# Kernel optimization log

Measured on AMD Instinct MI355X. Metric: run time of the kernel, lower is better.

Reference implementation:

```python
import jax, jax.numpy as jnp
import numpy as np

B, S, D = 2, 2048, 1024
H, DK = 16, 64
NUM_BUCKETS, MAX_DIST = 32, 128
EPS = 1e-6


def _relative_position_bucket(q_len, k_len):
    # T5 bidirectional relative position bucketing.
    ctx = jnp.arange(q_len)[:, None]
    mem = jnp.arange(k_len)[None, :]
    rel = mem - ctx  # [q, k]
    nb = NUM_BUCKETS // 2
    ret = (rel > 0).astype(jnp.int32) * nb
    n = jnp.abs(rel)
    max_exact = nb // 2
    is_small = n < max_exact
    n_safe = jnp.maximum(n, 1).astype(jnp.float32)
    val_large = max_exact + (
        jnp.log(n_safe / max_exact) / np.log(MAX_DIST / max_exact) * (nb - max_exact)
    ).astype(jnp.int32)
    val_large = jnp.minimum(val_large, nb - 1)
    return ret + jnp.where(is_small, n, val_large)  # [q, k] int32


def setup_inputs() -> dict:
    key = jax.random.key(0)
    ks = jax.random.split(key, 7)
    s = 0.02
    return {
        "hidden_states": jax.random.normal(ks[0], (B, S, D), jnp.float32),
        "ln_g": jnp.ones((D,), jnp.float32),
        "ln_b": jnp.zeros((D,), jnp.float32),
        "Wq": jax.random.normal(ks[1], (D, H * DK), jnp.float32) * s,
        "Wk": jax.random.normal(ks[2], (D, H * DK), jnp.float32) * s,
        "Wv": jax.random.normal(ks[3], (D, H * DK), jnp.float32) * s,
        "Wo": jax.random.normal(ks[4], (H * DK, D), jnp.float32) * s,
        "rel_bias": jax.random.normal(ks[5], (NUM_BUCKETS, H), jnp.float32) * s,
    }


def reference(hidden_states, ln_g, ln_b, Wq, Wk, Wv, Wo, rel_bias):
    b, s, d = hidden_states.shape
    # LayerNorm (nn.LayerNorm with affine, biased variance)
    mu = jnp.mean(hidden_states, axis=-1, keepdims=True)
    var = jnp.mean(jnp.square(hidden_states - mu), axis=-1, keepdims=True)
    normed = (hidden_states - mu) * jax.lax.rsqrt(var + EPS) * ln_g + ln_b
    # QKV projections (no bias), split heads
    q = (normed @ Wq).reshape(b, s, H, DK)
    k = (normed @ Wk).reshape(b, s, H, DK)
    v = (normed @ Wv).reshape(b, s, H, DK)
    # T5 attention: NO 1/sqrt(d) scaling; learned relative-position bias added to logits
    scores = jnp.einsum("bqhd,bkhd->bhqk", q, k)
    bucket = _relative_position_bucket(s, s)          # [s, s]
    bias = jnp.transpose(rel_bias[bucket], (2, 0, 1))  # [H, s, s]
    attn = jax.nn.softmax(scores + bias[None], axis=-1)
    ctx = jnp.einsum("bhqk,bkhd->bqhd", attn, v).reshape(b, s, H * DK)
    out = ctx @ Wo
    # residual (dropout is identity in eval)
    return hidden_states + out
```

## Files before the change

### kernel.cpp

```cpp
#include <hip/hip_runtime.h>
#include <hip/hip_bf16.h>
#include <math.h>

typedef __attribute__((__ext_vector_type__(8))) short bf16x8;
typedef __attribute__((__ext_vector_type__(4))) float f32x4;
typedef __attribute__((__ext_vector_type__(16))) float f32x16;
typedef __attribute__((__ext_vector_type__(4))) unsigned int u32x4;

#define B_ 2
#define S_ 2048
#define D_ 1024
#define H_ 16
#define DK_ 64
#define M_ (B_*S_)
#define N3_ 3072
#define BIAS_LEN 4096
#define M0_ 24.0f
#define L2E_ 1.4426950408889634f
#define KSTRIDE 66

__device__ __forceinline__ unsigned int cvtpk(float a, float b){
  unsigned int r;
  asm("v_cvt_pk_bf16_f32 %0, %1, %2" : "=v"(r) : "v"(a), "v"(b));
  return r;
}
__device__ __forceinline__ unsigned short f2bf(float f){
  unsigned int r;
  asm("v_cvt_pk_bf16_f32 %0, %1, %2" : "=v"(r) : "v"(f), "v"(f));
  return (unsigned short)r;
}
__device__ __forceinline__ float bf2f(unsigned short u){
  union{unsigned int i; float f;} v; v.i = ((unsigned int)u)<<16; return v.f;
}

__device__ __forceinline__ float fexp2(float x){
#if __has_builtin(__builtin_amdgcn_exp2f)
  return __builtin_amdgcn_exp2f(x);
#else
  return __expf(x * 0.6931471805599453f);
#endif
}

__device__ __forceinline__ f32x4 zero4(){
  f32x4 z; z[0]=0.f; z[1]=0.f; z[2]=0.f; z[3]=0.f; return z;
}

__device__ __forceinline__ f32x4 mfma16(bf16x8 a, bf16x8 b, f32x4 c){
  return __builtin_amdgcn_mfma_f32_16x16x32_bf16(a, b, c, 0, 0, 0);
}
__device__ __forceinline__ f32x16 mfma32(bf16x8 a, bf16x8 b, f32x16 c){
  return __builtin_amdgcn_mfma_f32_32x32x16_bf16(a, b, c, 0, 0, 0);
}

__device__ __forceinline__ void gload16(const void* g, void* l){
  __builtin_amdgcn_global_load_lds(
      (const __attribute__((address_space(1))) void*)g,
      (__attribute__((address_space(3))) void*)l, 16, 0, 0);
}

__global__ __launch_bounds__(256) void transpose_cast_kernel(
    const float* __restrict__ Wq, const float* __restrict__ Wk,
    const float* __restrict__ Wv, const float* __restrict__ Wo,
    unsigned short* __restrict__ Wcat_t, unsigned short* __restrict__ Wo_t)
{
  __shared__ float tile[64][65];
  const int k0 = blockIdx.x * 64;
  const int v0 = blockIdx.y * 64;
  const int sel = v0 >> 10;
  const float* W = (sel==0) ? Wq : (sel==1) ? Wk : (sel==2) ? Wv : Wo;
  const int nn0 = v0 & 1023;
  #pragma unroll
  for (int i=0;i<16;i++){
    int idx = i*256 + threadIdx.x;
    int r = idx >> 6, c = idx & 63;
    tile[r][c] = W[(size_t)(k0+r)*1024 + nn0 + c];
  }
  __syncthreads();
  #pragma unroll
  for (int i=0;i<16;i++){
    int idx = i*256 + threadIdx.x;
    int nr = idx >> 6, kc = idx & 63;
    unsigned short bv = f2bf(tile[kc][nr]);
    if (sel < 3) Wcat_t[(size_t)(v0+nr)*1024 + k0 + kc] = bv;
    else         Wo_t[(size_t)(v0-3072+nr)*1024 + k0 + kc] = bv;
  }
}

__global__ __launch_bounds__(256) void bias_tab_kernel(
    const float* __restrict__ rel_bias, float* __restrict__ biasTab)
{
  int t = blockIdx.x*256 + threadIdx.x;
  if (t >= H_*BIAS_LEN) return;
  int h = t / BIAS_LEN;
  int idx = t - h*BIAS_LEN;
  int rel = idx - (S_-1);
  int ret = (rel > 0) ? 16 : 0;
  int n = (rel < 0) ? -rel : rel;
  int bidx;
  if (n < 8) bidx = n;
  else {
    float vl = logf((float)n * 0.125f) / 2.7725887f * 8.0f;
    int v = 8 + (int)vl;
    bidx = (v < 15) ? v : 15;
  }
  biasTab[t] = (rel_bias[(ret + bidx)*H_ + h] - M0_) * L2E_;
}

__global__ __launch_bounds__(256) void ln_kernel(
    const float* __restrict__ x, const float* __restrict__ g,
    const float* __restrict__ bta, unsigned short* __restrict__ out)
{
  const int row = blockIdx.x;
  const int tid = threadIdx.x;
  float4 v = ((const float4*)(x + (size_t)row*D_))[tid];
  float s  = v.x+v.y+v.z+v.w;
  float ss = v.x*v.x+v.y*v.y+v.z*v.z+v.w*v.w;
  #pragma unroll
  for (int off=1; off<64; off<<=1){ s += __shfl_xor(s,off,64); ss += __shfl_xor(ss,off,64); }
  __shared__ float rs[4], rss[4];
  const int wid = tid >> 6, lane = tid & 63;
  if (lane == 0){ rs[wid] = s; rss[wid] = ss; }
  __syncthreads();
  s  = rs[0]+rs[1]+rs[2]+rs[3];
  ss = rss[0]+rss[1]+rss[2]+rss[3];
  float mu  = s * (1.0f/1024.0f);
  float var = ss * (1.0f/1024.0f) - mu*mu;
  float rstd = rsqrtf(var + 1e-6f);
  float4 gg = ((const float4*)g)[tid];
  float4 bb = ((const float4*)bta)[tid];
  uint2 o;
  o.x = cvtpk((v.x-mu)*rstd*gg.x + bb.x, (v.y-mu)*rstd*gg.y + bb.y);
  o.y = cvtpk((v.z-mu)*rstd*gg.z + bb.z, (v.w-mu)*rstd*gg.w + bb.w);
  ((uint2*)(out + (size_t)row*D_))[tid] = o;
}

template<int MODE>
__global__ __launch_bounds__(256) void gemm_kernel(
    const unsigned short* __restrict__ A,
    const unsigned short* __restrict__ Bt,
    const float* __restrict__ resid,
    unsigned short* __restrict__ Qb,
    unsigned short* __restrict__ Kb,
    unsigned short* __restrict__ Vtb,
    float* __restrict__ outf,
    int Ndim, int Kdim)
{
  __shared__ unsigned short As[128*64];
  __shared__ unsigned short Bs[128*64];
  const int tid = threadIdx.x;
  const int wid = tid >> 6, lane = tid & 63;
  const int lr = lane & 15, lg = lane >> 4;
  const int wm = (wid >> 1) * 64, wn = (wid & 1) * 64;

  const int nbx = gridDim.x;
  const int total = nbx * gridDim.y;
  const int flat = blockIdx.y * nbx + blockIdx.x;
  const int swz = (flat & 7) * (total >> 3) + (flat >> 3);
  const int m0 = (swz % nbx) * 128, n0 = (swz / nbx) * 128;

  f32x4 acc[4][4];
  #pragma unroll
  for (int i=0;i<4;i++)
    #pragma unroll
    for (int j=0;j<4;j++) acc[i][j] = zero4();

  for (int k0 = 0; k0 < Kdim; k0 += 64) {
    __syncthreads();
    #pragma unroll
    for (int i=0;i<4;i++){
      int c = i*256 + tid;
      int row = c >> 3, ch = c & 7;
      int chs = ch ^ (row & 7);
      gload16(A  + (size_t)(m0+row)*Kdim + k0 + chs*8, As + c*8);
      gload16(Bt + (size_t)(n0+row)*Kdim + k0 + chs*8, Bs + c*8);
    }
    __syncthreads();
    #pragma unroll
    for (int kk=0;kk<2;kk++){
      bf16x8 aF[4], bF[4];
      #pragma unroll
      for (int mi=0;mi<4;mi++){
        int row = wm + mi*16 + lr;
        aF[mi] = *(const bf16x8*)&As[row*64 + (((kk*4+lg) ^ (row & 7)) * 8)];
      }
      #pragma unroll
      for (int ni=0;ni<4;ni++){
        int row = wn + ni*16 + lr;
        bF[ni] = *(const bf16x8*)&Bs[row*64 + (((kk*4+lg) ^ (row & 7)) * 8)];
      }
      #pragma unroll
      for (int mi=0;mi<4;mi++)
        #pragma unroll
        for (int ni=0;ni<4;ni++)
          acc[mi][ni] = mfma16(aF[mi], bF[ni], acc[mi][ni]);
    }
  }

  if (MODE == 1) {
    #pragma unroll
    for (int mi=0;mi<4;mi++)
      #pragma unroll
      for (int ni=0;ni<4;ni++)
        #pragma unroll
        for (int r=0;r<4;r++){
          int m = m0 + wm + mi*16 + lg*4 + r;
          int n = n0 + wn + ni*16 + lr;
          outf[(size_t)m*Ndim + n] = acc[mi][ni][r] + resid[(size_t)m*Ndim + n];
        }
  } else {
    const int seln = n0 >> 10;
    if (seln == 2) {
      #pragma unroll
      for (int mi=0;mi<4;mi++)
        #pragma unroll
        for (int ni=0;ni<4;ni++){
          int m = m0 + wm + mi*16 + lg*4;
          int n = n0 + wn + ni*16 + lr;
          int nn = n & 1023, hh = nn >> 6, dk = nn & 63;
          int b = m >> 11, s = m & 2047;
          uint2 u;
          u.x = cvtpk(acc[mi][ni][0], acc[mi][ni][1]);
          u.y = cvtpk(acc[mi][ni][2], acc[mi][ni][3]);
          *(uint2*)(Vtb + (((size_t)(b*H_+hh))*DK_ + dk)*S_ + s) = u;
        }
    } else {
      unsigned short* __restrict__ dst = (seln == 0) ? Qb : Kb;
      #pragma unroll
      for (int mi=0;mi<4;mi++)
        #pragma unroll
        for (int ni=0;ni<4;ni++)
          #pragma unroll
          for (int r=0;r<4;r++){
            int m = m0 + wm + mi*16 + lg*4 + r;
            int n = n0 + wn + ni*16 + lr;
            int nn = n & 1023, hh = nn >> 6, dk = nn & 63;
            int b = m >> 11, s = m & 2047;
            dst[(((size_t)(b*H_+hh))*S_ + s)*DK_ + dk] = f2bf(acc[mi][ni][r]);
          }
    }
  }
}

#define SOFTMAX_PV(Svec, BG, UNIP, UNIN, VF00, VF01, VF10, VF11, ACC, LS)        \
{                                                                                \
  float p[16];                                                                   \
  if (UNIP) {                                                                    \
    _Pragma("unroll")                                                            \
    for (int r=0;r<16;r++) p[r] = fexp2(__builtin_fmaf(Svec[r], L2E_, cpos));    \
  } else if (UNIN) {                                                             \
    _Pragma("unroll")                                                            \
    for (int r=0;r<16;r++) p[r] = fexp2(__builtin_fmaf(Svec[r], L2E_, cneg));    \
  } else {                                                                       \
    _Pragma("unroll")                                                            \
    for (int r=0;r<16;r++){                                                      \
      int key = k0 + st*32 + (r&3) + 8*(r>>2) + 4*hi;                            \
      p[r] = fexp2(__builtin_fmaf(Svec[r], L2E_, BG[key]));                      \
    }                                                                            \
  }                                                                              \
                                       \
  {                                                                              \
    float t0=p[0]+p[1], t1=p[2]+p[3], t2=p[4]+p[5], t3=p[6]+p[7];                \
    float t4=p[8]+p[9], t5=p[10]+p[11], t6=p[12]+p[13], t7=p[14]+p[15];          \
    LS += ((t0+t1)+(t2+t3)) + ((t4+t5)+(t6+t7));                                 \
  }                                                                              \
  unsigned int W00=cvtpk(p[0],p[1]),  W01=cvtpk(p[4],p[5]);                      \
  unsigned int W02=cvtpk(p[8],p[9]),  W03=cvtpk(p[12],p[13]);                    \
  unsigned int W10=cvtpk(p[2],p[3]),  W11=cvtpk(p[6],p[7]);                      \
  unsigned int W12=cvtpk(p[10],p[11]),W13=cvtpk(p[14],p[15]);                    \
  unsigned int X00=__shfl_xor(W00,32), X01=__shfl_xor(W01,32);                   \
  unsigned int X02=__shfl_xor(W02,32), X03=__shfl_xor(W03,32);                   \
  unsigned int X10=__shfl_xor(W10,32), X11=__shfl_xor(W11,32);                   \
  unsigned int X12=__shfl_xor(W12,32), X13=__shfl_xor(W13,32);                   \
  u32x4 pu0; u32x4 pu1;                                                          \
  pu0[0] = hi ? X01 : W00;  pu0[1] = hi ? X11 : W10;                             \
  pu0[2] = hi ? W01 : X00;  pu0[3] = hi ? W11 : X10;                             \
  pu1[0] = hi ? X03 : W02;  pu1[1] = hi ? X13 : W12;                             \
  pu1[2] = hi ? W03 : X02;  pu1[3] = hi ? W13 : X12;                             \
  bf16x8 pav0 = __builtin_bit_cast(bf16x8, pu0);                                 \
  bf16x8 pav1 = __builtin_bit_cast(bf16x8, pu1);                                 \
  ACC[0] = mfma32(pav0, VF00, ACC[0]);                                           \
  ACC[1] = mfma32(pav0, VF01, ACC[1]);                                           \
  ACC[0] = mfma32(pav1, VF10, ACC[0]);                                           \
  ACC[1] = mfma32(pav1, VF11, ACC[1]);                                           \
}

__global__ __launch_bounds__(256, 2) void attn_kernel(
    const unsigned short* __restrict__ Qb,
    const unsigned short* __restrict__ Kb,
    const unsigned short* __restrict__ Vtb,
    const float* __restrict__ biasTab,
    const float* __restrict__ rel_bias,
    unsigned short* __restrict__ Opart,
    float* __restrict__ Lpart)
{
  __shared__ unsigned short Ks[64*KSTRIDE];
  __shared__ unsigned short Vts[64*KSTRIDE];

  const int tid = threadIdx.x;
  const int wid = tid >> 6, lane = tid & 63;
  const int ql = lane & 31;
  const int hi = lane >> 5;

  const int flat = (blockIdx.z * 32 + blockIdx.y) * 8 + blockIdx.x;
  const int wf = (flat & 7) * 64 + (flat >> 3);
  const int qt = wf & 7;
  const int bh = (wf >> 3) & 31;
  const int kg = wf >> 8;

  const int h = bh & (H_-1);
  const int b = bh >> 4;
  const int kbase = kg << 10;
  const int q0w = qt*256 + wid*64;

  const float cpos = (rel_bias[31*H_ + h] - M0_) * L2E_;
  const float cneg = (rel_bias[15*H_ + h] - M0_) * L2E_;
  const float* bGa = biasTab + (size_t)h*BIAS_LEN + 2047 - (q0w + ql);
  const float* bGb = bGa - 32;

  const unsigned short* Qpa = Qb + ((size_t)bh*S_ + q0w + ql)*DK_;
  bf16x8 qfa[4], qfb[4];
  #pragma unroll
  for (int c=0;c<4;c++){
    qfa[c] = *(const bf16x8*)(Qpa + 16*c + 8*hi);
    qfb[c] = *(const bf16x8*)(Qpa + 32*DK_ + 16*c + 8*hi);
  }

  const unsigned short* Ksrc = Kb  + (size_t)bh*S_*DK_;
  const unsigned short* Vsrc = Vtb + (size_t)bh*DK_*S_;
  const int c0 = tid, c1 = tid + 256;
  const int r0 = c0 >> 3, ch0 = c0 & 7;
  const int r1 = c1 >> 3, ch1 = c1 & 7;

  f32x16 acca[2], accb[2];
  #pragma unroll
  for (int i=0;i<16;i++){ acca[0][i]=0.f; acca[1][i]=0.f; accb[0][i]=0.f; accb[1][i]=0.f; }
  float lsa = 0.f, lsb = 0.f;

  bf16x8 sk0 = *(const bf16x8*)(Ksrc + (size_t)(kbase + r0)*DK_ + ch0*8);
  bf16x8 sk1 = *(const bf16x8*)(Ksrc + (size_t)(kbase + r1)*DK_ + ch1*8);
  bf16x8 sv0 = *(const bf16x8*)(Vsrc + (size_t)r0*S_ + kbase + ch0*8);
  bf16x8 sv1 = *(const bf16x8*)(Vsrc + (size_t)r1*S_ + kbase + ch1*8);

  for (int k0 = kbase; k0 < kbase + 1024; k0 += 64) {
    __syncthreads();
    *(bf16x8*)&Ks [r0*KSTRIDE + ch0*8] = sk0;
    *(bf16x8*)&Ks [r1*KSTRIDE + ch1*8] = sk1;
    *(bf16x8*)&Vts[r0*KSTRIDE + ch0*8] = sv0;
    *(bf16x8*)&Vts[r1*KSTRIDE + ch1*8] = sv1;
    __syncthreads();
    if (k0 + 64 < kbase + 1024) {
      int kn = k0 + 64;
      sk0 = *(const bf16x8*)(Ksrc + (size_t)(kn + r0)*DK_ + ch0*8);
      sk1 = *(const bf16x8*)(Ksrc + (size_t)(kn + r1)*DK_ + ch1*8);
      sv0 = *(const bf16x8*)(Vsrc + (size_t)r0*S_ + kn + ch0*8);
      sv1 = *(const bf16x8*)(Vsrc + (size_t)r1*S_ + kn + ch1*8);
    }

    const bool upa = (k0 >= q0w + 122),      una = (k0 <= q0w - 154);
    const bool upb = (k0 >= q0w + 32 + 122), unb = (k0 <= q0w + 32 - 154);

    #pragma unroll
    for (int st=0; st<2; ++st){
      const int arow = st*32 + ql;
      bf16x8 kf0 = *(const bf16x8*)&Ks[arow*KSTRIDE + (0+hi)*8];
      bf16x8 kf1 = *(const bf16x8*)&Ks[arow*KSTRIDE + (2+hi)*8];
      bf16x8 kf2 = *(const bf16x8*)&Ks[arow*KSTRIDE + (4+hi)*8];
      bf16x8 kf3 = *(const bf16x8*)&Ks[arow*KSTRIDE + (6+hi)*8];

      f32x16 sa, sb;
      #pragma unroll
      for (int i=0;i<16;i++){ sa[i]=0.f; sb[i]=0.f; }
      sa = mfma32(kf0, qfa[0], sa); sb = mfma32(kf0, qfb[0], sb);
      sa = mfma32(kf1, qfa[1], sa); sb = mfma32(kf1, qfb[1], sb);
      sa = mfma32(kf2, qfa[2], sa); sb = mfma32(kf2, qfb[2], sb);
      sa = mfma32(kf3, qfa[3], sa); sb = mfma32(kf3, qfb[3], sb);

      bf16x8 vf00 = *(const bf16x8*)&Vts[(ql     )*KSTRIDE + (4*st+  hi)*8];
      bf16x8 vf01 = *(const bf16x8*)&Vts[(ql + 32)*KSTRIDE + (4*st+  hi)*8];
      bf16x8 vf10 = *(const bf16x8*)&Vts[(ql     )*KSTRIDE + (4*st+2+hi)*8];
      bf16x8 vf11 = *(const bf16x8*)&Vts[(ql + 32)*KSTRIDE + (4*st+2+hi)*8];

      SOFTMAX_PV(sa, bGa, upa, una, vf00, vf01, vf10, vf11, acca, lsa);
      SOFTMAX_PV(sb, bGb, upb, unb, vf00, vf01, vf10, vf11, accb, lsb);
    }
  }

  float lta = lsa + __shfl_xor(lsa, 32);
  float ltb = lsb + __shfl_xor(lsb, 32);
  if (hi == 0) {
    Lpart[((size_t)kg*B_*H_ + bh)*S_ + q0w + ql]      = lta;
    Lpart[((size_t)kg*B_*H_ + bh)*S_ + q0w + 32 + ql] = ltb;
  }
  #pragma unroll
  for (int r=0;r<16;r++){
    const int qr = (r&3) + 8*(r>>2) + 4*hi;
    #pragma unroll
    for (int dt=0; dt<2; ++dt){
      const int d = ql + 32*dt;
      Opart[(size_t)kg*M_*D_ + ((size_t)(b*S_ + q0w + qr)*H_ + h)*DK_ + d]      = f2bf(acca[dt][r]);
      Opart[(size_t)kg*M_*D_ + ((size_t)(b*S_ + q0w + 32 + qr)*H_ + h)*DK_ + d] = f2bf(accb[dt][r]);
    }
  }
}

__global__ __launch_bounds__(256) void combine_kernel(
    const unsigned short* __restrict__ Opart, const float* __restrict__ Lpart,
    unsigned short* __restrict__ ctxb)
{
  const int t = blockIdx.x*256 + threadIdx.x;
  const int f = t*8;
  const int qgl = f >> 10;
  const int h = (f >> 6) & 15;
  const int bh = (qgl >> 11)*H_ + h;
  const int s = qgl & 2047;
  const float l0 = Lpart[(size_t)bh*S_ + s];
  const float l1 = Lpart[(size_t)B_*H_*S_ + (size_t)bh*S_ + s];
  const float linv = 1.0f / (l0 + l1);
  bf16x8 p0 = *(const bf16x8*)(Opart + f);
  bf16x8 p1 = *(const bf16x8*)(Opart + (size_t)M_*D_ + f);
  u32x4 o;
  #pragma unroll
  for (int j=0;j<4;j++){
    float a = (bf2f((unsigned short)p0[2*j+0]) + bf2f((unsigned short)p1[2*j+0])) * linv;
    float c = (bf2f((unsigned short)p0[2*j+1]) + bf2f((unsigned short)p1[2*j+1])) * linv;
    o[j] = cvtpk(a, c);
  }
  *(u32x4*)(ctxb + f) = o;
}

extern "C" void kernel_launch(void* const* d_in, const int* in_sizes, int n_in,
                              void* d_out, int out_size, void* d_ws, size_t ws_size,
                              hipStream_t stream) {
  const float* hidden   = (const float*)d_in[0];
  const float* ln_g     = (const float*)d_in[1];
  const float* ln_b     = (const float*)d_in[2];
  const float* Wq       = (const float*)d_in[3];
  const float* Wk       = (const float*)d_in[4];
  const float* Wv       = (const float*)d_in[5];
  const float* Wo       = (const float*)d_in[6];
  const float* rel_bias = (const float*)d_in[7];
  float* out = (float*)d_out;

  char* ws = (char*)d_ws;
  const size_t off_ln   = 0;
  const size_t off_wcat = 8388608;
  const size_t off_q    = 16777216;
  const size_t off_k    = 25165824;
  const size_t off_vt   = 33554432;
  const size_t off_ctx  = 41943040;
  const size_t off_bias = 50331648;
  const size_t off_lp   = 50593792;
  const size_t off_wo   = 51118080;

  unsigned short* ln_out  = (unsigned short*)(ws + off_ln);
  unsigned short* Wcat_t  = (unsigned short*)(ws + off_wcat);
  unsigned short* Wo_t    = (unsigned short*)(ws + off_wo);
  unsigned short* Qb      = (unsigned short*)(ws + off_q);
  unsigned short* Kb      = (unsigned short*)(ws + off_k);
  unsigned short* Vtb     = (unsigned short*)(ws + off_vt);
  unsigned short* ctxb    = (unsigned short*)(ws + off_ctx);
  float*          biasTab = (float*)(ws + off_bias);
  float*          Lpart   = (float*)(ws + off_lp);
  unsigned short* Opart   = (unsigned short*)(ws + 0);

  transpose_cast_kernel<<<dim3(16,64), 256, 0, stream>>>(Wq, Wk, Wv, Wo, Wcat_t, Wo_t);
  bias_tab_kernel<<<(H_*BIAS_LEN + 255)/256, 256, 0, stream>>>(rel_bias, biasTab);
  ln_kernel<<<M_, 256, 0, stream>>>(hidden, ln_g, ln_b, ln_out);
  gemm_kernel<0><<<dim3(M_/128, N3_/128), 256, 0, stream>>>(
      ln_out, Wcat_t, nullptr, Qb, Kb, Vtb, nullptr, N3_, D_);
  attn_kernel<<<dim3(8, 32, 2), 256, 0, stream>>>(
      Qb, Kb, Vtb, biasTab, rel_bias, Opart, Lpart);
  combine_kernel<<<(M_*D_/8)/256, 256, 0, stream>>>(Opart, Lpart, ctxb);
  gemm_kernel<1><<<dim3(M_/128, D_/128), 256, 0, stream>>>(
      ctxb, Wo_t, hidden, nullptr, nullptr, nullptr, out, D_, D_);
}
```

Baseline: 141.6 us.

## Fuse split-K attention combine into output projection GEMM A-tile load

```diff
diff --git a/kernel.cpp b/kernel.cpp
--- a/kernel.cpp
+++ b/kernel.cpp
@@ -134,16 +134,12 @@
   ((uint2*)(out + (size_t)row*D_))[tid] = o;
 }
 
-template<int MODE>
-__global__ __launch_bounds__(256) void gemm_kernel(
+__global__ __launch_bounds__(256) void gemm_qkv_kernel(
     const unsigned short* __restrict__ A,
     const unsigned short* __restrict__ Bt,
-    const float* __restrict__ resid,
     unsigned short* __restrict__ Qb,
     unsigned short* __restrict__ Kb,
-    unsigned short* __restrict__ Vtb,
-    float* __restrict__ outf,
-    int Ndim, int Kdim)
+    unsigned short* __restrict__ Vtb)
 {
   __shared__ unsigned short As[128*64];
   __shared__ unsigned short Bs[128*64];
@@ -164,15 +160,15 @@
     #pragma unroll
     for (int j=0;j<4;j++) acc[i][j] = zero4();
 
-  for (int k0 = 0; k0 < Kdim; k0 += 64) {
+  for (int k0 = 0; k0 < D_; k0 += 64) {
     __syncthreads();
     #pragma unroll
     for (int i=0;i<4;i++){
       int c = i*256 + tid;
       int row = c >> 3, ch = c & 7;
       int chs = ch ^ (row & 7);
-      gload16(A  + (size_t)(m0+row)*Kdim + k0 + chs*8, As + c*8);
-      gload16(Bt + (size_t)(n0+row)*Kdim + k0 + chs*8, Bs + c*8);
+      gload16(A  + (size_t)(m0+row)*D_ + k0 + chs*8, As + c*8);
+      gload16(Bt + (size_t)(n0+row)*D_ + k0 + chs*8, Bs + c*8);
     }
     __syncthreads();
     #pragma unroll
@@ -196,7 +192,23 @@
     }
   }
 
-  if (MODE == 1) {
+  const int seln = n0 >> 10;
+  if (seln == 2) {
+    #pragma unroll
+    for (int mi=0;mi<4;mi++)
+      #pragma unroll
+      for (int ni=0;ni<4;ni++){
+        int m = m0 + wm + mi*16 + lg*4;
+        int n = n0 + wn + ni*16 + lr;
+        int nn = n & 1023, hh = nn >> 6, dk = nn & 63;
+        int b = m >> 11, s = m & 2047;
+        uint2 u;
+        u.x = cvtpk(acc[mi][ni][0], acc[mi][ni][1]);
+        u.y = cvtpk(acc[mi][ni][2], acc[mi][ni][3]);
+        *(uint2*)(Vtb + (((size_t)(b*H_+hh))*DK_ + dk)*S_ + s) = u;
+      }
+  } else {
+    unsigned short* __restrict__ dst = (seln == 0) ? Qb : Kb;
     #pragma unroll
     for (int mi=0;mi<4;mi++)
       #pragma unroll
@@ -205,39 +217,10 @@
         for (int r=0;r<4;r++){
           int m = m0 + wm + mi*16 + lg*4 + r;
           int n = n0 + wn + ni*16 + lr;
-          outf[(size_t)m*Ndim + n] = acc[mi][ni][r] + resid[(size_t)m*Ndim + n];
-        }
-  } else {
-    const int seln = n0 >> 10;
-    if (seln == 2) {
-      #pragma unroll
-      for (int mi=0;mi<4;mi++)
-        #pragma unroll
-        for (int ni=0;ni<4;ni++){
-          int m = m0 + wm + mi*16 + lg*4;
-          int n = n0 + wn + ni*16 + lr;
           int nn = n & 1023, hh = nn >> 6, dk = nn & 63;
           int b = m >> 11, s = m & 2047;
-          uint2 u;
-          u.x = cvtpk(acc[mi][ni][0], acc[mi][ni][1]);
-          u.y = cvtpk(acc[mi][ni][2], acc[mi][ni][3]);
-          *(uint2*)(Vtb + (((size_t)(b*H_+hh))*DK_ + dk)*S_ + s) = u;
+          dst[(((size_t)(b*H_+hh))*S_ + s)*DK_ + dk] = f2bf(acc[mi][ni][r]);
         }
-    } else {
-      unsigned short* __restrict__ dst = (seln == 0) ? Qb : Kb;
-      #pragma unroll
-      for (int mi=0;mi<4;mi++)
-        #pragma unroll
-        for (int ni=0;ni<4;ni++)
-          #pragma unroll
-          for (int r=0;r<4;r++){
-            int m = m0 + wm + mi*16 + lg*4 + r;
-            int n = n0 + wn + ni*16 + lr;
-            int nn = n & 1023, hh = nn >> 6, dk = nn & 63;
-            int b = m >> 11, s = m & 2047;
-            dst[(((size_t)(b*H_+hh))*S_ + s)*DK_ + dk] = f2bf(acc[mi][ni][r]);
-          }
-    }
   }
 }
 
@@ -403,29 +386,96 @@
   }
 }
 
-__global__ __launch_bounds__(256) void combine_kernel(
-    const unsigned short* __restrict__ Opart, const float* __restrict__ Lpart,
-    unsigned short* __restrict__ ctxb)
+__global__ __launch_bounds__(256) void gemm_out_kernel(
+    const unsigned short* __restrict__ Opart,
+    const float* __restrict__ Lpart,
+    const unsigned short* __restrict__ Wo_t,
+    const float* __restrict__ resid,
+    float* __restrict__ outf)
 {
-  const int t = blockIdx.x*256 + threadIdx.x;
-  const int f = t*8;
-  const int qgl = f >> 10;
-  const int h = (f >> 6) & 15;
-  const int bh = (qgl >> 11)*H_ + h;
-  const int s = qgl & 2047;
-  const float l0 = Lpart[(size_t)bh*S_ + s];
-  const float l1 = Lpart[(size_t)B_*H_*S_ + (size_t)bh*S_ + s];
-  const float linv = 1.0f / (l0 + l1);
-  bf16x8 p0 = *(const bf16x8*)(Opart + f);
-  bf16x8 p1 = *(const bf16x8*)(Opart + (size_t)M_*D_ + f);
-  u32x4 o;
-  #pragma unroll
-  for (int j=0;j<4;j++){
-    float a = (bf2f((unsigned short)p0[2*j+0]) + bf2f((unsigned short)p1[2*j+0])) * linv;
-    float c = (bf2f((unsigned short)p0[2*j+1]) + bf2f((unsigned short)p1[2*j+1])) * linv;
-    o[j] = cvtpk(a, c);
-  }
-  *(u32x4*)(ctxb + f) = o;
+  __shared__ unsigned short As[64*64];
+  __shared__ unsigned short Bs[128*64];
+  const int tid = threadIdx.x;
+  const int wid = tid >> 6, lane = tid & 63;
+  const int lr = lane & 15, lg = lane >> 4;
+  const int wm = (wid & 1) * 32, wn = (wid >> 1) * 64;
+
+  const int nbx = gridDim.x;
+  const int total = nbx * gridDim.y;
+  const int flat = blockIdx.y * nbx + blockIdx.x;
+  const int swz = (flat & 7) * (total >> 3) + (flat >> 3);
+  const int m0 = (swz % nbx) * 64, n0 = (swz / nbx) * 128;
+
+  f32x4 acc[2][4];
+  #pragma unroll
+  for (int i=0;i<2;i++)
+    #pragma unroll
+    for (int j=0;j<4;j++) acc[i][j] = zero4();
+
+  for (int k0 = 0; k0 < D_; k0 += 64) {
+    const int hh = k0 >> 6;
+    __syncthreads();
+    #pragma unroll
+    for (int i=0;i<4;i++){
+      int c = i*256 + tid;
+      int row = c >> 3, ch = c & 7;
+      int chs = ch ^ (row & 7);
+      gload16(Wo_t + (size_t)(n0+row)*D_ + k0 + chs*8, Bs + c*8);
+    }
+    #pragma unroll
+    for (int i=0;i<2;i++){
+      int c = i*256 + tid;
+      int row = c >> 3, ch = c & 7;
+      int m = m0 + row;
+      int bb = m >> 11, s = m & 2047;
+      int bhh = bb*H_ + hh;
+      float l0 = Lpart[(size_t)bhh*S_ + s];
+      float l1 = Lpart[(size_t)B_*H_*S_ + (size_t)bhh*S_ + s];
+      float li = 1.0f / (l0 + l1);
+      size_t addr = (size_t)m*D_ + k0 + ch*8;
+      bf16x8 p0 = *(const bf16x8*)(Opart + addr);
+      bf16x8 p1 = *(const bf16x8*)(Opart + (size_t)M_*D_ + addr);
+      u32x4 o;
+      #pragma unroll
+      for (int j=0;j<4;j++){
+        float a = (bf2f((unsigned short)p0[2*j+0]) + bf2f((unsigned short)p1[2*j+0])) * li;
+        float cc= (bf2f((unsigned short)p0[2*j+1]) + bf2f((unsigned short)p1[2*j+1])) * li;
+        o[j] = cvtpk(a, cc);
+      }
+      *(u32x4*)&As[row*64 + ((ch ^ (row & 7))*8)] = o;
+    }
+    __syncthreads();
+    #pragma unroll
+    for (int kk=0;kk<2;kk++){
+      bf16x8 aF[2], bF[4];
+      #pragma unroll
+      for (int mi=0;mi<2;mi++){
+        int row = wm + mi*16 + lr;
+        aF[mi] = *(const bf16x8*)&As[row*64 + (((kk*4+lg) ^ (row & 7)) * 8)];
+      }
+      #pragma unroll
+      for (int ni=0;ni<4;ni++){
+        int row = wn + ni*16 + lr;
+        bF[ni] = *(const bf16x8*)&Bs[row*64 + (((kk*4+lg) ^ (row & 7)) * 8)];
+      }
+      #pragma unroll
+      for (int mi=0;mi<2;mi++)
+        #pragma unroll
+        for (int ni=0;ni<4;ni++)
+          acc[mi][ni] = mfma16(aF[mi], bF[ni], acc[mi][ni]);
+    }
+  }
+
+  #pragma unroll
+  for (int mi=0;mi<2;mi++)
+    #pragma unroll
+    for (int ni=0;ni<4;ni++)
+      #pragma unroll
+      for (int r=0;r<4;r++){
+        int m = m0 + wm + mi*16 + lg*4 + r;
+        int n = n0 + wn + ni*16 + lr;
+        outf[(size_t)m*D_ + n] = acc[mi][ni][r] + resid[(size_t)m*D_ + n];
+      }
 }
 
 extern "C" void kernel_launch(void* const* d_in, const int* in_sizes, int n_in,
@@ -447,7 +497,6 @@
   const size_t off_q    = 16777216;
   const size_t off_k    = 25165824;
   const size_t off_vt   = 33554432;
-  const size_t off_ctx  = 41943040;
   const size_t off_bias = 50331648;
   const size_t off_lp   = 50593792;
   const size_t off_wo   = 51118080;
@@ -458,7 +507,6 @@
   unsigned short* Qb      = (unsigned short*)(ws + off_q);
   unsigned short* Kb      = (unsigned short*)(ws + off_k);
   unsigned short* Vtb     = (unsigned short*)(ws + off_vt);
-  unsigned short* ctxb    = (unsigned short*)(ws + off_ctx);
   float*          biasTab = (float*)(ws + off_bias);
   float*          Lpart   = (float*)(ws + off_lp);
   unsigned short* Opart   = (unsigned short*)(ws + 0);
@@ -466,11 +514,10 @@
   transpose_cast_kernel<<<dim3(16,64), 256, 0, stream>>>(Wq, Wk, Wv, Wo, Wcat_t, Wo_t);
   bias_tab_kernel<<<(H_*BIAS_LEN + 255)/256, 256, 0, stream>>>(rel_bias, biasTab);
   ln_kernel<<<M_, 256, 0, stream>>>(hidden, ln_g, ln_b, ln_out);
-  gemm_kernel<0><<<dim3(M_/128, N3_/128), 256, 0, stream>>>(
-      ln_out, Wcat_t, nullptr, Qb, Kb, Vtb, nullptr, N3_, D_);
+  gemm_qkv_kernel<<<dim3(M_/128, N3_/128), 256, 0, stream>>>(
+      ln_out, Wcat_t, Qb, Kb, Vtb);
   attn_kernel<<<dim3(8, 32, 2), 256, 0, stream>>>(
       Qb, Kb, Vtb, biasTab, rel_bias, Opart, Lpart);
-  combine_kernel<<<(M_*D_/8)/256, 256, 0, stream>>>(Opart, Lpart, ctxb);
-  gemm_kernel<1><<<dim3(M_/128, D_/128), 256, 0, stream>>>(
-      ctxb, Wo_t, hidden, nullptr, nullptr, nullptr, out, D_, D_);
-}
+  gemm_out_kernel<<<dim3(M_/64, D_/128), 256, 0, stream>>>(
+      Opart, Lpart, Wo_t, hidden, out);
+}
```

New measurement: 140.6 us. Within noise of the previous version (-0.7%).
